# Kernel optimization log

Hardware: AMD Instinct MI355X
Metric: run time of the kernel (lower is better)

## Reference

```python
import jax, jax.numpy as jnp
import numpy as np

EOS = 1e-10
ALPHA = 0.5
TEMPERATURE = 1.0
BIAS = 0.0001
N_NODES = 8192
N_EDGES = 262144
INPUT_DIM = 512
HIDDEN = 128


def setup_inputs() -> dict:
    key = jax.random.key(0)
    ks = jax.random.split(key, 7)
    features = jax.random.normal(ks[0], (N_NODES, INPUT_DIM), dtype=jnp.float32)
    W_emb = jax.random.normal(ks[1], (HIDDEN, INPUT_DIM), dtype=jnp.float32) * (1.0 / np.sqrt(INPUT_DIM))
    b_emb = jax.random.normal(ks[2], (HIDDEN,), dtype=jnp.float32) * 0.01
    W_edge = jax.random.normal(ks[3], (1, 2 * HIDDEN), dtype=jnp.float32) * (1.0 / np.sqrt(2 * HIDDEN))
    b_edge = jax.random.normal(ks[4], (1,), dtype=jnp.float32) * 0.01
    noise = jax.random.uniform(ks[5], (N_EDGES,), dtype=jnp.float32)
    edges = jax.random.randint(ks[6], (2, N_EDGES), 0, N_NODES, dtype=jnp.int64 if jax.config.jax_enable_x64 else jnp.int32)
    return {"features": features, "W_emb": W_emb, "b_emb": b_emb,
            "W_edge": W_edge, "b_edge": b_edge, "noise": noise, "edges": edges}


def _sym_normalize(adj):
    # inv_sqrt_degree[:,None] * adj * inv_sqrt_degree[None,:]
    inv_sqrt_deg = 1.0 / (jnp.sqrt(adj.sum(axis=1)) + EOS)
    return adj * inv_sqrt_deg[:, None] * inv_sqrt_deg[None, :]


def reference(features, W_emb, b_emb, W_edge, b_edge, noise, edges):
    n = N_NODES
    # node embedding: single Linear + ReLU
    h = jax.nn.relu(features @ W_emb.T + b_emb)            # [N, H]
    e0, e1 = edges[0], edges[1]
    h0, h1 = h[e0], h[e1]                                   # [E, H] gathers
    Wa, Wb = W_edge[0, :HIDDEN], W_edge[0, HIDDEN:]
    s1 = h0 @ Wa + h1 @ Wb + b_edge[0]                       # edge_mlp(cat(h0,h1))
    s2 = h1 @ Wa + h0 @ Wb + b_edge[0]                       # edge_mlp(cat(h1,h0))
    raw = 0.5 * (s1 + s2)                                    # [E]
    # gumbel gate: eps = (bias-(1-bias))*rand + (1-bias)
    eps = (BIAS - (1.0 - BIAS)) * noise + (1.0 - BIAS)
    gate = (jnp.log(eps) - jnp.log1p(-eps) + raw) / TEMPERATURE
    weights_lp = jax.nn.sigmoid(gate)                        # [E]
    weights_hp = 1.0 - weights_lp
    eye = jnp.eye(n, dtype=features.dtype)
    # scatter edge weights to dense adjacency (assignment semantics, like torch adj[e0,e1]=w)
    adj_lp = jnp.zeros((n, n), dtype=features.dtype).at[e0, e1].set(weights_lp) + eye
    adj_lp = _sym_normalize(adj_lp)
    adj_hp = jnp.zeros((n, n), dtype=features.dtype).at[e0, e1].set(weights_hp) + eye
    adj_hp = _sym_normalize(adj_hp)
    mask = jnp.zeros((n, n), dtype=features.dtype).at[e0, e1].set(1.0)
    adj_hp = eye - adj_hp * mask * ALPHA
    return (adj_lp, adj_hp, weights_lp, weights_hp)
```

## Files before the change

### kernel.cpp

```cpp
#include <hip/hip_runtime.h>
#include <cstdint>
#include <cstddef>

#define N_NODES 8192
#define N_EDGES 262144
#define INPUT_DIM 512
#define HIDDEN 128
#define ALPHA 0.5f
#define EOS 1e-10f
#define BCAP 128

#define BK 32
#define BM 32

typedef float v4 __attribute__((ext_vector_type(4)));

__global__ __launch_bounds__(512) void k1_g(
    const float* __restrict__ F, const float* __restrict__ W,
    const float* __restrict__ bemb, const float* __restrict__ Wedge,
    float* __restrict__ g)
{
    __shared__ float Fl[BK][BM + 1];
    __shared__ float Wl[BK][HIDDEN + 4];
    int tid = threadIdx.x;
    int tx = tid & 15;
    int ty = tid >> 4;
    int node0 = blockIdx.x * BM;

    float acc[8];
#pragma unroll
    for (int j = 0; j < 8; j++) acc[j] = 0.f;

    for (int d0 = 0; d0 < INPUT_DIM; d0 += BK) {
        if (tid < 256) {
            int r = tid >> 3, dd = (tid & 7) << 2;
            float4 v = *(const float4*)&F[(size_t)(node0 + r) * INPUT_DIM + d0 + dd];
            Fl[dd + 0][r] = v.x; Fl[dd + 1][r] = v.y;
            Fl[dd + 2][r] = v.z; Fl[dd + 3][r] = v.w;
        }
#pragma unroll
        for (int i = 0; i < 2; i++) {
            int idx = tid + i * 512;
            int kr = idx >> 3, dd = (idx & 7) << 2;
            float4 v = *(const float4*)&W[(size_t)kr * INPUT_DIM + d0 + dd];
            Wl[dd + 0][kr] = v.x; Wl[dd + 1][kr] = v.y;
            Wl[dd + 2][kr] = v.z; Wl[dd + 3][kr] = v.w;
        }
        __syncthreads();
#pragma unroll
        for (int kk = 0; kk < BK; kk++) {
            float f0 = Fl[kk][ty];
            float4 wA = *(float4*)&Wl[kk][tx * 8];
            float4 wB = *(float4*)&Wl[kk][tx * 8 + 4];
            acc[0] = fmaf(f0, wA.x, acc[0]);
            acc[1] = fmaf(f0, wA.y, acc[1]);
            acc[2] = fmaf(f0, wA.z, acc[2]);
            acc[3] = fmaf(f0, wA.w, acc[3]);
            acc[4] = fmaf(f0, wB.x, acc[4]);
            acc[5] = fmaf(f0, wB.y, acc[5]);
            acc[6] = fmaf(f0, wB.z, acc[6]);
            acc[7] = fmaf(f0, wB.w, acc[7]);
        }
        __syncthreads();
    }
    float s = 0.f;
#pragma unroll
    for (int j = 0; j < 8; j++) {
        int k = tx * 8 + j;
        float h = acc[j] + bemb[k];
        h = h > 0.f ? h : 0.f;
        s += h * (Wedge[k] + Wedge[HIDDEN + k]);
    }
#pragma unroll
    for (int off = 8; off > 0; off >>= 1)
        s += __shfl_down(s, off, 16);
    if (tx == 0) g[node0 + ty] = s;
}

__global__ __launch_bounds__(256) void k_edge(
    const int* __restrict__ edges, const float* __restrict__ noise,
    const float* __restrict__ g, const float* __restrict__ bedge,
    float* __restrict__ wlp, float* __restrict__ whp,
    int* __restrict__ cnt, int* __restrict__ bucket)
{
    int i = blockIdx.x * 256 + threadIdx.x;
    int e0 = edges[i], e1 = edges[N_EDGES + i];
    float raw = 0.5f * (g[e0] + g[e1]) + bedge[0];
    float eps = -0.9998f * noise[i] + 0.9999f;
    float gate = logf(eps) - log1pf(-eps) + raw;
    float w = 1.f / (1.f + expf(-gate));
    wlp[i] = w;
    whp[i] = 1.f - w;
    int pos = atomicAdd(&cnt[e0], 1);
    if (pos < BCAP) bucket[e0 * BCAP + pos] = i;
}

__global__ __launch_bounds__(256) void k_deginv(
    const int* __restrict__ edges, const float* __restrict__ wlp,
    const float* __restrict__ whp,
    const int* __restrict__ cnt, const int* __restrict__ bucket,
    float* __restrict__ inv_lp, float* __restrict__ inv_hp)
{
    __shared__ int cols[BCAP];
    __shared__ int eidx[BCAP];
    __shared__ float s_lp[256], s_hp[256];
    int r = blockIdx.x;
    int tid = threadIdx.x;
    int d = cnt[r];
    if (d > BCAP) d = BCAP;
    if (tid < d) {
        int i = bucket[r * BCAP + tid];
        eidx[tid] = i;
        cols[tid] = edges[N_EDGES + i];
    }
    __syncthreads();
    float plp = 0.f, php = 0.f;
    if (tid < d) {
        int c = cols[tid], i = eidx[tid];
        bool win = true;
        for (int j = 0; j < d; j++)
            if (cols[j] == c && eidx[j] > i) win = false;
        if (win) { plp = wlp[i]; php = whp[i]; }
    }
    s_lp[tid] = plp; s_hp[tid] = php;
    __syncthreads();
    for (int off = 128; off; off >>= 1) {
        if (tid < off) { s_lp[tid] += s_lp[tid + off]; s_hp[tid] += s_hp[tid + off]; }
        __syncthreads();
    }
    if (tid == 0) {
        inv_lp[r] = 1.f / (sqrtf(s_lp[0] + 1.f) + EOS);
        inv_hp[r] = 1.f / (sqrtf(s_hp[0] + 1.f) + EOS);
    }
}

__global__ __launch_bounds__(256) void k_fill(
    const int* __restrict__ edges, const float* __restrict__ wlp,
    const float* __restrict__ whp,
    const int* __restrict__ cnt, const int* __restrict__ bucket,
    const float* __restrict__ inv_lp, const float* __restrict__ inv_hp,
    float* __restrict__ LP, float* __restrict__ HP)
{
    __shared__ float row[N_NODES];
    __shared__ int cols[BCAP];
    __shared__ int eidx[BCAP];
    __shared__ float wv[BCAP];
    int b = blockIdx.x;
    int m = b & 1;
    int r = b >> 1;
    int tid = threadIdx.x;
    v4* rv = (v4*)row;
#pragma unroll
    for (int i = 0; i < 8; i++) rv[tid + i * 256] = 0.f;

    int d = cnt[r];
    if (d > BCAP) d = BCAP;
    const float* wsrc = m ? whp : wlp;
    const float* isrc = m ? inv_hp : inv_lp;
    if (tid < d) {
        int i = bucket[r * BCAP + tid];
        eidx[tid] = i;
        cols[tid] = edges[N_EDGES + i];
        wv[tid] = wsrc[i];
    }
    float ir = isrc[r];
    __syncthreads();
    if (tid == 0) row[r] = m ? 1.0f : ir * ir;
    __syncthreads();
    if (tid < d) {
        int c = cols[tid], i = eidx[tid];
        bool win = true;
        for (int j = 0; j < d; j++)
            if (cols[j] == c && eidx[j] > i) win = false;
        if (win) {
            float ic = isrc[c];
            float diag = (c == r) ? 1.f : 0.f;
            row[c] = m ? (diag - (wv[tid] + diag) * ir * ic * ALPHA)
                       : ((wv[tid] + diag) * ir * ic);
        }
    }
    __syncthreads();
    v4* dst = (v4*)((m ? HP : LP) + (size_t)r * N_NODES);
#pragma unroll
    for (int i = 0; i < 8; i++)
        __builtin_nontemporal_store(rv[tid + i * 256], &dst[tid + i * 256]);
}

extern "C" void kernel_launch(void* const* d_in, const int* in_sizes, int n_in,
                              void* d_out, int out_size, void* d_ws, size_t ws_size,
                              hipStream_t stream) {
    const float* F     = (const float*)d_in[0];
    const float* W     = (const float*)d_in[1];
    const float* bemb  = (const float*)d_in[2];
    const float* Wedge = (const float*)d_in[3];
    const float* bedge = (const float*)d_in[4];
    const float* noise = (const float*)d_in[5];
    const int*   edges = (const int*)d_in[6];

    const size_t N2 = (size_t)N_NODES * N_NODES;
    float* out = (float*)d_out;
    float* LP  = out;
    float* HP  = out + N2;
    float* wlp = HP + N2;
    float* whp = wlp + N_EDGES;

    char* ws = (char*)d_ws;
    float* g      = (float*)(ws);
    int*   cnt    = (int*)  (ws + 32768);
    float* inv_lp = (float*)(ws + 65536);
    float* inv_hp = (float*)(ws + 98304);
    int*   bucket = (int*)  (ws + 131072);

    hipMemsetAsync(cnt, 0, N_NODES * sizeof(int), stream);

    k1_g<<<N_NODES / BM, 512, 0, stream>>>(F, W, bemb, Wedge, g);
    k_edge<<<N_EDGES / 256, 256, 0, stream>>>(edges, noise, g, bedge,
                                              wlp, whp, cnt, bucket);
    k_deginv<<<N_NODES, 256, 0, stream>>>(edges, wlp, whp, cnt, bucket,
                                          inv_lp, inv_hp);
    k_fill<<<2 * N_NODES, 256, 0, stream>>>(edges, wlp, whp, cnt, bucket,
                                            inv_lp, inv_hp, LP, HP);
}
```

Measured before the change: 625.0 us.

## Use bf16 MFMA for embedding GEMM and precompute dedup winners in deginv

Several unrelated changes. The node-embedding GEMM now converts inputs to bf16 in shared memory and uses 16x16x32 MFMA instructions in place of scalar FP32 FMAs, with a wave-shuffle reduction to produce g. The cnt memset moves into k1_g. k_deginv processes two rows per block with shuffle reductions and writes packed (col,edge) winners back into the bucket, so k_fill no longer repeats the O(d^2) duplicate scan or the edges gather. The output kernel writes 2x256 MB dense matrices and dominates runtime, so these upstream savings touch a small fraction of total time; bf16 also lowers the precision of the embedding.

```diff
diff --git a/kernel.cpp b/kernel.cpp
--- a/kernel.cpp
+++ b/kernel.cpp
@@ -9,72 +9,88 @@
 #define ALPHA 0.5f
 #define EOS 1e-10f
 #define BCAP 128
-
-#define BK 32
-#define BM 32
+#define LDA 40
 
 typedef float v4 __attribute__((ext_vector_type(4)));
-
-__global__ __launch_bounds__(512) void k1_g(
+typedef __attribute__((ext_vector_type(8))) short short8;
+typedef __attribute__((ext_vector_type(4))) float floatx4;
+
+__device__ inline unsigned short f2bf(float x) {
+    unsigned u = __builtin_bit_cast(unsigned, x);
+    return (unsigned short)((u + 0x7FFFu + ((u >> 16) & 1u)) >> 16);
+}
+__device__ inline unsigned pack2(float a, float b) {
+    return (unsigned)f2bf(a) | ((unsigned)f2bf(b) << 16);
+}
+
+__global__ __launch_bounds__(128) void k1_g(
     const float* __restrict__ F, const float* __restrict__ W,
     const float* __restrict__ bemb, const float* __restrict__ Wedge,
-    float* __restrict__ g)
-{
-    __shared__ float Fl[BK][BM + 1];
-    __shared__ float Wl[BK][HIDDEN + 4];
+    float* __restrict__ g, int* __restrict__ cnt)
+{
+    __shared__ unsigned short As[32 * LDA];
+    __shared__ unsigned short Bs[128 * LDA];
     int tid = threadIdx.x;
-    int tx = tid & 15;
-    int ty = tid >> 4;
-    int node0 = blockIdx.x * BM;
-
-    float acc[8];
-#pragma unroll
-    for (int j = 0; j < 8; j++) acc[j] = 0.f;
-
-    for (int d0 = 0; d0 < INPUT_DIM; d0 += BK) {
-        if (tid < 256) {
-            int r = tid >> 3, dd = (tid & 7) << 2;
-            float4 v = *(const float4*)&F[(size_t)(node0 + r) * INPUT_DIM + d0 + dd];
-            Fl[dd + 0][r] = v.x; Fl[dd + 1][r] = v.y;
-            Fl[dd + 2][r] = v.z; Fl[dd + 3][r] = v.w;
+    int gt = blockIdx.x * 128 + tid;
+    if (gt < N_NODES) cnt[gt] = 0;
+
+    int node0 = blockIdx.x * 32;
+    int lane = tid & 63, wave = tid >> 6;
+    int ml = lane & 15, q = lane >> 4;
+
+    floatx4 acc[8];
+#pragma unroll
+    for (int f = 0; f < 8; f++) acc[f] = 0.f;
+
+    for (int s = 0; s < 16; s++) {
+        int d0 = s * 32;
+#pragma unroll
+        for (int j = 0; j < 2; j++) {
+            int qi = j * 128 + tid;
+            int row = qi >> 3, dq = (qi & 7) * 4;
+            float4 v = *(const float4*)&F[(size_t)(node0 + row) * INPUT_DIM + d0 + dq];
+            uint2 p; p.x = pack2(v.x, v.y); p.y = pack2(v.z, v.w);
+            *(uint2*)&As[row * LDA + dq] = p;
         }
 #pragma unroll
-        for (int i = 0; i < 2; i++) {
-            int idx = tid + i * 512;
-            int kr = idx >> 3, dd = (idx & 7) << 2;
-            float4 v = *(const float4*)&W[(size_t)kr * INPUT_DIM + d0 + dd];
-            Wl[dd + 0][kr] = v.x; Wl[dd + 1][kr] = v.y;
-            Wl[dd + 2][kr] = v.z; Wl[dd + 3][kr] = v.w;
+        for (int j = 0; j < 8; j++) {
+            int qi = j * 128 + tid;
+            int row = qi >> 3, dq = (qi & 7) * 4;
+            float4 v = *(const float4*)&W[(size_t)row * INPUT_DIM + d0 + dq];
+            uint2 p; p.x = pack2(v.x, v.y); p.y = pack2(v.z, v.w);
+            *(uint2*)&Bs[row * LDA + dq] = p;
         }
         __syncthreads();
-#pragma unroll
-        for (int kk = 0; kk < BK; kk++) {
-            float f0 = Fl[kk][ty];
-            float4 wA = *(float4*)&Wl[kk][tx * 8];
-            float4 wB = *(float4*)&Wl[kk][tx * 8 + 4];
-            acc[0] = fmaf(f0, wA.x, acc[0]);
-            acc[1] = fmaf(f0, wA.y, acc[1]);
-            acc[2] = fmaf(f0, wA.z, acc[2]);
-            acc[3] = fmaf(f0, wA.w, acc[3]);
-            acc[4] = fmaf(f0, wB.x, acc[4]);
-            acc[5] = fmaf(f0, wB.y, acc[5]);
-            acc[6] = fmaf(f0, wB.z, acc[6]);
-            acc[7] = fmaf(f0, wB.w, acc[7]);
+        short8 a = *(const short8*)&As[(wave * 16 + ml) * LDA + q * 8];
+#pragma unroll
+        for (int f = 0; f < 8; f++) {
+            short8 b = *(const short8*)&Bs[(f * 16 + ml) * LDA + q * 8];
+            acc[f] = __builtin_amdgcn_mfma_f32_16x16x32_bf16(a, b, acc[f], 0, 0, 0);
         }
         __syncthreads();
     }
-    float s = 0.f;
-#pragma unroll
-    for (int j = 0; j < 8; j++) {
-        int k = tx * 8 + j;
-        float h = acc[j] + bemb[k];
-        h = h > 0.f ? h : 0.f;
-        s += h * (Wedge[k] + Wedge[HIDDEN + k]);
-    }
-#pragma unroll
-    for (int off = 8; off > 0; off >>= 1)
-        s += __shfl_down(s, off, 16);
-    if (tx == 0) g[node0 + ty] = s;
+    float s0 = 0.f, s1 = 0.f, s2 = 0.f, s3 = 0.f;
+#pragma unroll
+    for (int f = 0; f < 8; f++) {
+        int n = f * 16 + ml;
+        float u = Wedge[n] + Wedge[HIDDEN + n];
+        float bb = bemb[n];
+        float h0 = acc[f][0] + bb; s0 += (h0 > 0.f ? h0 : 0.f) * u;
+        float h1 = acc[f][1] + bb; s1 += (h1 > 0.f ? h1 : 0.f) * u;
+        float h2 = acc[f][2] + bb; s2 += (h2 > 0.f ? h2 : 0.f) * u;
+        float h3 = acc[f][3] + bb; s3 += (h3 > 0.f ? h3 : 0.f) * u;
+    }
+#pragma unroll
+    for (int m = 1; m < 16; m <<= 1) {
+        s0 += __shfl_xor(s0, m, 64);
+        s1 += __shfl_xor(s1, m, 64);
+        s2 += __shfl_xor(s2, m, 64);
+        s3 += __shfl_xor(s3, m, 64);
+    }
+    if (ml == 0) {
+        int node = node0 + wave * 16 + q * 4;
+        g[node + 0] = s0; g[node + 1] = s1; g[node + 2] = s2; g[node + 3] = s3;
+    }
 }
 
 __global__ __launch_bounds__(256) void k_edge(
@@ -97,87 +113,76 @@
 
 __global__ __launch_bounds__(256) void k_deginv(
     const int* __restrict__ edges, const float* __restrict__ wlp,
-    const float* __restrict__ whp,
-    const int* __restrict__ cnt, const int* __restrict__ bucket,
-    float* __restrict__ inv_lp, float* __restrict__ inv_hp)
-{
-    __shared__ int cols[BCAP];
-    __shared__ int eidx[BCAP];
-    __shared__ float s_lp[256], s_hp[256];
-    int r = blockIdx.x;
+    const float* __restrict__ whp, const int* __restrict__ cnt,
+    int* __restrict__ bucket, float* __restrict__ inv_lp, float* __restrict__ inv_hp)
+{
+    __shared__ int cols[2][BCAP];
+    __shared__ int eidx[2][BCAP];
+    __shared__ float plp[4], php[4];
     int tid = threadIdx.x;
-    int d = cnt[r];
-    if (d > BCAP) d = BCAP;
-    if (tid < d) {
-        int i = bucket[r * BCAP + tid];
-        eidx[tid] = i;
-        cols[tid] = edges[N_EDGES + i];
-    }
-    __syncthreads();
-    float plp = 0.f, php = 0.f;
-    if (tid < d) {
-        int c = cols[tid], i = eidx[tid];
+    int half = tid >> 7, lt = tid & 127;
+    int r = blockIdx.x * 2 + half;
+    int d = cnt[r]; if (d > BCAP) d = BCAP;
+    int i = -1, c = -1;
+    if (lt < d) {
+        i = bucket[r * BCAP + lt];
+        c = edges[N_EDGES + i];
+        cols[half][lt] = c;
+        eidx[half][lt] = i;
+    }
+    __syncthreads();
+    float sl = 0.f, sh = 0.f;
+    if (lt < d) {
         bool win = true;
         for (int j = 0; j < d; j++)
-            if (cols[j] == c && eidx[j] > i) win = false;
-        if (win) { plp = wlp[i]; php = whp[i]; }
-    }
-    s_lp[tid] = plp; s_hp[tid] = php;
-    __syncthreads();
-    for (int off = 128; off; off >>= 1) {
-        if (tid < off) { s_lp[tid] += s_lp[tid + off]; s_hp[tid] += s_hp[tid + off]; }
-        __syncthreads();
-    }
-    if (tid == 0) {
-        inv_lp[r] = 1.f / (sqrtf(s_lp[0] + 1.f) + EOS);
-        inv_hp[r] = 1.f / (sqrtf(s_hp[0] + 1.f) + EOS);
+            if (cols[half][j] == c && eidx[half][j] > i) { win = false; break; }
+        int packv = -1;
+        if (win) { sl = wlp[i]; sh = whp[i]; packv = (c << 18) | i; }
+        bucket[r * BCAP + lt] = packv;
+    }
+#pragma unroll
+    for (int m = 1; m < 64; m <<= 1) {
+        sl += __shfl_xor(sl, m, 64);
+        sh += __shfl_xor(sh, m, 64);
+    }
+    int wv = tid >> 6;
+    if ((tid & 63) == 0) { plp[wv] = sl; php[wv] = sh; }
+    __syncthreads();
+    if (lt == 0) {
+        float l = plp[half * 2] + plp[half * 2 + 1];
+        float h = php[half * 2] + php[half * 2 + 1];
+        inv_lp[r] = 1.f / (sqrtf(l + 1.f) + EOS);
+        inv_hp[r] = 1.f / (sqrtf(h + 1.f) + EOS);
     }
 }
 
 __global__ __launch_bounds__(256) void k_fill(
-    const int* __restrict__ edges, const float* __restrict__ wlp,
-    const float* __restrict__ whp,
+    const float* __restrict__ wlp, const float* __restrict__ whp,
     const int* __restrict__ cnt, const int* __restrict__ bucket,
     const float* __restrict__ inv_lp, const float* __restrict__ inv_hp,
     float* __restrict__ LP, float* __restrict__ HP)
 {
     __shared__ float row[N_NODES];
-    __shared__ int cols[BCAP];
-    __shared__ int eidx[BCAP];
-    __shared__ float wv[BCAP];
-    int b = blockIdx.x;
-    int m = b & 1;
-    int r = b >> 1;
-    int tid = threadIdx.x;
+    int b = blockIdx.x, m = b & 1, r = b >> 1, tid = threadIdx.x;
     v4* rv = (v4*)row;
 #pragma unroll
     for (int i = 0; i < 8; i++) rv[tid + i * 256] = 0.f;
 
-    int d = cnt[r];
-    if (d > BCAP) d = BCAP;
+    int d = cnt[r]; if (d > BCAP) d = BCAP;
     const float* wsrc = m ? whp : wlp;
     const float* isrc = m ? inv_hp : inv_lp;
-    if (tid < d) {
-        int i = bucket[r * BCAP + tid];
-        eidx[tid] = i;
-        cols[tid] = edges[N_EDGES + i];
-        wv[tid] = wsrc[i];
-    }
     float ir = isrc[r];
+    int pv = -1;
+    if (tid < d) pv = bucket[r * BCAP + tid];
     __syncthreads();
     if (tid == 0) row[r] = m ? 1.0f : ir * ir;
     __syncthreads();
-    if (tid < d) {
-        int c = cols[tid], i = eidx[tid];
-        bool win = true;
-        for (int j = 0; j < d; j++)
-            if (cols[j] == c && eidx[j] > i) win = false;
-        if (win) {
-            float ic = isrc[c];
-            float diag = (c == r) ? 1.f : 0.f;
-            row[c] = m ? (diag - (wv[tid] + diag) * ir * ic * ALPHA)
-                       : ((wv[tid] + diag) * ir * ic);
-        }
+    if (pv >= 0) {
+        int c = pv >> 18, i = pv & 0x3FFFF;
+        float w = wsrc[i], ic = isrc[c];
+        float diag = (c == r) ? 1.f : 0.f;
+        row[c] = m ? (diag - (w + diag) * ir * ic * ALPHA)
+                   : ((w + diag) * ir * ic);
     }
     __syncthreads();
     v4* dst = (v4*)((m ? HP : LP) + (size_t)r * N_NODES);
@@ -211,13 +216,11 @@
     float* inv_hp = (float*)(ws + 98304);
     int*   bucket = (int*)  (ws + 131072);
 
-    hipMemsetAsync(cnt, 0, N_NODES * sizeof(int), stream);
-
-    k1_g<<<N_NODES / BM, 512, 0, stream>>>(F, W, bemb, Wedge, g);
+    k1_g<<<256, 128, 0, stream>>>(F, W, bemb, Wedge, g, cnt);
     k_edge<<<N_EDGES / 256, 256, 0, stream>>>(edges, noise, g, bedge,
                                               wlp, whp, cnt, bucket);
-    k_deginv<<<N_NODES, 256, 0, stream>>>(edges, wlp, whp, cnt, bucket,
-                                          inv_lp, inv_hp);
-    k_fill<<<2 * N_NODES, 256, 0, stream>>>(edges, wlp, whp, cnt, bucket,
+    k_deginv<<<N_NODES / 2, 256, 0, stream>>>(edges, wlp, whp, cnt, bucket,
+                                              inv_lp, inv_hp);
+    k_fill<<<2 * N_NODES, 256, 0, stream>>>(wlp, whp, cnt, bucket,
                                             inv_lp, inv_hp, LP, HP);
 }
```

After: 648.4 us. 3.7% more time.
